# Kernel tuning notes

Hardware: AMD Instinct MI355X
Metric: run time of the kernel (lower is better)

## Reference

```python
import jax, jax.numpy as jnp
import numpy as np

EPS = 1e-5
SLOPE = 0.01  # LeakyReLU default negative_slope


def conv3(x, w):
    # x: [B,C,D,H,W], w: [O,I,3,3,3]; SubMConv3d on a dense grid == dense SAME conv, no bias
    return jax.lax.conv_general_dilated(
        x, w, window_strides=(1, 1, 1), padding='SAME',
        dimension_numbers=('NCDHW', 'OIDHW', 'NCDHW'))


def bn_c(x, g, b, m, v):
    # BatchNorm1d (eval) over channel axis 1 of [B,C,D,H,W]
    s = (1.0, -1, 1, 1, 1)
    return (x - m.reshape(1, -1, 1, 1, 1)) * (g.reshape(1, -1, 1, 1, 1) * jax.lax.rsqrt(v.reshape(1, -1, 1, 1, 1) + EPS)) + b.reshape(1, -1, 1, 1, 1)


def bn_f(x, g, b, m, v):
    # BatchNorm1d (eval) over last (feature) axis
    return (x - m) * (g * jax.lax.rsqrt(v + EPS)) + b


def lrelu(x):
    return jnp.where(x > 0, x, SLOPE * x)


def setup_inputs() -> dict:
    key = jax.random.key(0)
    ks = jax.random.split(key, 32)
    B, C, D, H, W = 2, 256, 64, 64, 16
    N = 100000
    init_size, emb = 32, 3

    fea = jax.random.normal(ks[0], (B, C, D, H, W), dtype=jnp.float32)
    gi0 = jax.random.randint(ks[1], (B, N), 0, D)
    gi1 = jax.random.randint(ks[2], (B, N), 0, H)
    gi2 = jax.random.randint(ks[3], (B, N), 0, W)
    grid_ind = jnp.stack([gi0, gi1, gi2], axis=-1).astype(jnp.int32)  # [B,N,3]
    xyz = jax.random.normal(ks[4], (B, N, 3), dtype=jnp.float32)

    def bn_params(k, c):
        k1, k2, k3, k4 = jax.random.split(k, 4)
        return (1.0 + 0.1 * jax.random.normal(k1, (c,), jnp.float32),
                0.1 * jax.random.normal(k2, (c,), jnp.float32),
                0.1 * jax.random.normal(k3, (c,), jnp.float32),
                0.5 + jax.random.uniform(k4, (c,), jnp.float32))

    W1 = jax.random.normal(ks[5], (C, C, 3, 3, 3), jnp.float32) * (1.0 / np.sqrt(27 * C))
    g1, b1, m1, v1 = bn_params(ks[6], C)
    W2 = jax.random.normal(ks[7], (2 * init_size, C, 3, 3, 3), jnp.float32) * (1.0 / np.sqrt(27 * C))
    g2, b2, m2, v2 = bn_params(ks[8], 2 * init_size)
    W3 = jax.random.normal(ks[9], (init_size, 2 * init_size, 3, 3, 3), jnp.float32) * (1.0 / np.sqrt(27 * 2 * init_size))
    g3, b3, m3, v3 = bn_params(ks[10], init_size)

    Wo1 = jax.random.normal(ks[11], (init_size + 3, init_size), jnp.float32) * (1.0 / np.sqrt(init_size + 3))
    bo1 = 0.01 * jax.random.normal(ks[12], (init_size,), jnp.float32)
    go, bo, mo, vo = bn_params(ks[13], init_size)
    Wo2 = jax.random.normal(ks[14], (init_size, emb), jnp.float32) * (1.0 / np.sqrt(init_size))
    bo2 = 0.01 * jax.random.normal(ks[15], (emb,), jnp.float32)

    return dict(fea=fea, grid_ind=grid_ind, xyz=xyz,
                W1=W1, g1=g1, b1=b1, m1=m1, v1=v1,
                W2=W2, g2=g2, b2=b2, m2=m2, v2=v2,
                W3=W3, g3=g3, b3=b3, m3=m3, v3=v3,
                Wo1=Wo1, bo1=bo1, go=go, bo=bo, mo=mo, vo=vo,
                Wo2=Wo2, bo2=bo2)


def reference(fea, grid_ind, xyz,
              W1, g1, b1, m1, v1,
              W2, g2, b2, m2, v2,
              W3, g3, b3, m3, v3,
              Wo1, bo1, go, bo, mo, vo,
              Wo2, bo2):
    # sparse conv stack (dense-grid equivalent)
    x = lrelu(bn_c(conv3(fea, W1), g1, b1, m1, v1))
    x = lrelu(bn_c(conv3(x, W2), g2, b2, m2, v2))
    x = lrelu(bn_c(conv3(x, W3), g3, b3, m3, v3))  # [B, init_size, D, H, W]

    # fea.dense().permute(0,2,3,4,1) -> [B, D, H, W, C]; per-point gather
    xg = jnp.transpose(x, (0, 2, 3, 4, 1))
    B = xg.shape[0]
    bidx = jnp.arange(B)[:, None]  # [B,1]
    pt = xg[bidx, grid_ind[:, :, 0], grid_ind[:, :, 1], grid_ind[:, :, 2]]  # [B, N, init_size]

    # concat xyz, Linear -> BN -> ReLU -> Linear
    h = jnp.concatenate([pt, xyz[:, :, :3]], axis=-1)
    h = jax.nn.relu(bn_f(h @ Wo1 + bo1, go, bo, mo, vo))
    return h @ Wo2 + bo2  # [B, N, embedding_dim]
```

## Files before the change

kernel.cpp:

```cpp
#include <hip/hip_runtime.h>
#include <stdint.h>

#define EPS 1e-5f
#define SLOPE 0.01f

typedef short bf16x8 __attribute__((ext_vector_type(8)));
typedef float f32x4 __attribute__((ext_vector_type(4)));

__device__ __forceinline__ uint16_t f2bf(float x) {
  union { float f; uint32_t u; } v; v.f = x;
  return (uint16_t)((v.u + 0x7fffu + ((v.u >> 16) & 1u)) >> 16);
}

__device__ __forceinline__ void g2lds16(const void* g, void* l) {
  __builtin_amdgcn_global_load_lds(
      (const __attribute__((address_space(1))) void*)g,
      (__attribute__((address_space(3))) void*)l, 16, 0, 0);
}

__global__ void prep_bn(const float* g1, const float* b1, const float* m1, const float* v1,
                        const float* g2, const float* b2, const float* m2, const float* v2,
                        const float* g3, const float* b3, const float* m3, const float* v3,
                        const float* go, const float* bo, const float* mo, const float* vo,
                        const float* bo1,
                        float* s1, float* be1, float* s2, float* be2,
                        float* s3, float* be3, float* so, float* beo) {
  int t = threadIdx.x;
  if (t < 256) { float s = g1[t] / sqrtf(v1[t] + EPS); s1[t] = s; be1[t] = b1[t] - m1[t] * s; }
  if (t < 64)  { float s = g2[t] / sqrtf(v2[t] + EPS); s2[t] = s; be2[t] = b2[t] - m2[t] * s; }
  if (t < 32)  { float s = g3[t] / sqrtf(v3[t] + EPS); s3[t] = s; be3[t] = b3[t] - m3[t] * s; }
  if (t < 32)  { float s = go[t] / sqrtf(vo[t] + EPS); so[t] = s; beo[t] = bo[t] + (bo1[t] - mo[t]) * s; }
}

__global__ void wtrans(const float* __restrict__ W, uint16_t* __restrict__ Wt,
                       int CO, int CI) {
  int idx = blockIdx.x * 256 + threadIdx.x;
  int total = CO * CI * 27;
  if (idx >= total) return;
  int t = idx / (CO * CI);
  int rem = idx % (CO * CI);
  int co = rem / CI, ci = rem % CI;
  Wt[idx] = f2bf(W[((size_t)co * CI + ci) * 27 + t]);
}

__global__ __launch_bounds__(256) void transpose_fea(const float* __restrict__ fea,
                                                     uint16_t* __restrict__ pad0) {
  int tid = threadIdx.x;
  int idx = blockIdx.x;
  int half = idx & 1;
  int q = (idx >> 1) & 3;
  int d = (idx >> 3) & 63;
  int b = idx >> 9;
  int s = q * 256 + tid;
  int h = s >> 4, w = s & 15;
  const float* src = fea + (size_t)(b * 256 + half * 128) * 65536 + (size_t)d * 1024 + s;
  uint16_t* dst = pad0 + ((size_t)b * 78408 +
                          (size_t)((d + 1) * 1188 + (h + 1) * 18 + (w + 1))) * 256 + half * 128;
#pragma unroll 4
  for (int c8 = 0; c8 < 16; ++c8) {
    uint16_t v[8];
#pragma unroll
    for (int j = 0; j < 8; ++j)
      v[j] = f2bf(src[(size_t)(c8 * 8 + j) * 65536]);
    *(uint4*)&dst[c8 * 8] = *(uint4*)v;
  }
}

template <int CI, int CO, int MH, int WM, int WN, bool LAST>
__global__ __launch_bounds__(256, 2) void conv_mfma(const uint16_t* __restrict__ padIn,
                                                    const uint16_t* __restrict__ Wt,
                                                    const float* __restrict__ bnS,
                                                    const float* __restrict__ bnB,
                                                    uint16_t* __restrict__ padOut,
                                                    float* __restrict__ x3out) {
  constexpr int NTILE = CO;
  constexpr int MTILE = MH * 16;
  constexpr int MPW = MTILE / WM;
  constexpr int NPW = NTILE / WN;
  constexpr int MSUB = MPW / 16;
  constexpr int NSUB = NPW / 16;
  constexpr int BPASS = NTILE / 32;
  constexpr int KC = CI / 64;
  constexpr int HB = 64 / MH;
  constexpr int HALF = MH / 8;
  constexpr int ROWSTR = 18 * CI;

  __shared__ __align__(16) uint16_t Alds[20 * MH * 64];
  __shared__ __align__(16) uint16_t Blds[NTILE * 64];

  const int tid = threadIdx.x;
  const int lane = tid & 63;
  const int wv = tid >> 6;
  const int wvm = wv / WN;
  const int wvn = wv % WN;

  const int mt = blockIdx.x;
  const int b = mt / (64 * HB);
  const int r = mt % (64 * HB);
  const int d = r / HB;
  const int h0 = (r % HB) * MH;

  const int subswB = (tid & 7) ^ ((tid >> 3) & 7);
  const int rowB0 = tid >> 3;

  f32x4 acc[MSUB][NSUB] = {};

  const size_t bOffIn = (size_t)b * 78408 * CI;

  for (int dh = 0; dh < 9; ++dh) {
    const int kd = dh / 3, kh = dh % 3;
    const size_t Abase = bOffIn + (size_t)((d + kd) * 1188 + (h0 + kh) * 18) * CI;
    for (int kc = 0; kc < KC; ++kc) {
      for (int kw = 0; kw < 3; ++kw) {
        __syncthreads();
        if (kw == 0) {
          const uint16_t* agBase = padIn + Abase + kc * 64 + (size_t)(lane >> 3) * ROWSTR;
#pragma unroll
          for (int p = 0; p < 5; ++p) {
            int wp = wv * 5 + p;
            int gu = (lane & 7) ^ (wp & 7);
#pragma unroll
            for (int hf = 0; hf < HALF; ++hf)
              g2lds16(agBase + (size_t)(hf * 8) * ROWSTR + wp * CI + gu * 8,
                      (char*)Alds + wp * (MH * 128) + hf * 1024);
          }
        }
        {
          const uint16_t* bg = Wt + (size_t)((dh * 3 + kw) * CO) * CI + kc * 64 + subswB * 8;
#pragma unroll
          for (int p = 0; p < BPASS; ++p)
            g2lds16(bg + (size_t)(rowB0 + 32 * p) * CI, (char*)Blds + p * 4096 + wv * 1024);
        }
        __syncthreads();
#pragma unroll
        for (int ks = 0; ks < 2; ++ks) {
          bf16x8 af[MSUB], bfr[NSUB];
#pragma unroll
          for (int mi = 0; mi < MSUB; ++mi) {
            int wq = (lane & 15) + kw;
            int u = (ks * 4 + (lane >> 4)) ^ (wq & 7);
            int mhIdx = wvm * MSUB + mi;
            af[mi] = *(const bf16x8*)&Alds[wq * (MH * 64) + mhIdx * 64 + u * 8];
          }
#pragma unroll
          for (int ni = 0; ni < NSUB; ++ni) {
            int row = wvn * NPW + ni * 16 + (lane & 15);
            int u = (ks * 4 + (lane >> 4)) ^ (row & 7);
            bfr[ni] = *(const bf16x8*)&Blds[row * 64 + u * 8];
          }
#pragma unroll
          for (int mi = 0; mi < MSUB; ++mi)
#pragma unroll
            for (int ni = 0; ni < NSUB; ++ni)
              acc[mi][ni] = __builtin_amdgcn_mfma_f32_16x16x32_bf16(af[mi], bfr[ni], acc[mi][ni], 0, 0, 0);
        }
      }
    }
  }

  const int col = lane & 15;
  const int quad = lane >> 4;
#pragma unroll
  for (int ni = 0; ni < NSUB; ++ni) {
    const int co = wvn * NPW + ni * 16 + col;
    const float sv = bnS[co];
    const float bv = bnB[co];
#pragma unroll
    for (int mi = 0; mi < MSUB; ++mi) {
#pragma unroll
      for (int rr = 0; rr < 4; ++rr) {
        int m = wvm * MPW + mi * 16 + quad * 4 + rr;
        float v = acc[mi][ni][rr] * sv + bv;
        v = v > 0.f ? v : SLOPE * v;
        int mh = m >> 4, w = m & 15;
        if (!LAST) {
          size_t o = ((size_t)b * 78408 +
                      (size_t)((d + 1) * 1188 + (h0 + mh + 1) * 18 + (w + 1))) * CO + co;
          padOut[o] = f2bf(v);
        } else {
          size_t o = ((size_t)b * 65536 + (size_t)((d * 64 + h0 + mh) * 16 + w)) * 32 + co;
          x3out[o] = v;
        }
      }
    }
  }
}

__global__ __launch_bounds__(256) void gather_mlp(const float* __restrict__ x3,
                                                  const int* __restrict__ gidx,
                                                  const float* __restrict__ xyz,
                                                  const float* __restrict__ Wo1,
                                                  const float* __restrict__ so,
                                                  const float* __restrict__ beo,
                                                  const float* __restrict__ Wo2,
                                                  const float* __restrict__ bo2,
                                                  float* __restrict__ out) {
  __shared__ __align__(16) float w1[35 * 32];
  __shared__ float w2[32 * 3];
  __shared__ float sS[32], sB[32], b2s[3];
  int tid = threadIdx.x;
  for (int i = tid; i < 1120; i += 256) w1[i] = Wo1[i];
  if (tid < 96) w2[tid] = Wo2[tid];
  if (tid < 32) { sS[tid] = so[tid]; sB[tid] = beo[tid]; }
  if (tid < 3) b2s[tid] = bo2[tid];
  __syncthreads();

  int idx = blockIdx.x * 256 + tid;
  if (idx >= 200000) return;
  int b = idx >= 100000 ? 1 : 0;
  int gb = idx * 3;
  int i0 = gidx[gb], i1 = gidx[gb + 1], i2 = gidx[gb + 2];
  const float* pt = x3 + ((size_t)b * 65536 + (size_t)((i0 * 64 + i1) * 16 + i2)) * 32;

  float h[35];
#pragma unroll
  for (int q = 0; q < 8; ++q) {
    float4 v = *(const float4*)(pt + q * 4);
    h[q * 4] = v.x; h[q * 4 + 1] = v.y; h[q * 4 + 2] = v.z; h[q * 4 + 3] = v.w;
  }
  h[32] = xyz[gb]; h[33] = xyz[gb + 1]; h[34] = xyz[gb + 2];

  float a[32];
#pragma unroll
  for (int j = 0; j < 32; ++j) a[j] = 0.f;
#pragma unroll
  for (int k = 0; k < 35; ++k) {
    float hk = h[k];
    const float4* wr = (const float4*)(w1 + k * 32);
#pragma unroll
    for (int q = 0; q < 8; ++q) {
      float4 wv = wr[q];
      a[q * 4 + 0] += hk * wv.x;
      a[q * 4 + 1] += hk * wv.y;
      a[q * 4 + 2] += hk * wv.z;
      a[q * 4 + 3] += hk * wv.w;
    }
  }
  float o0 = b2s[0], o1 = b2s[1], o2 = b2s[2];
#pragma unroll
  for (int j = 0; j < 32; ++j) {
    float y = a[j] * sS[j] + sB[j];
    y = y > 0.f ? y : 0.f;
    o0 += y * w2[j * 3 + 0];
    o1 += y * w2[j * 3 + 1];
    o2 += y * w2[j * 3 + 2];
  }
  out[gb] = o0; out[gb + 1] = o1; out[gb + 2] = o2;
}

extern "C" void kernel_launch(void* const* d_in, const int* in_sizes, int n_in,
                              void* d_out, int out_size, void* d_ws, size_t ws_size,
                              hipStream_t stream) {
  (void)in_sizes; (void)n_in; (void)out_size;
  if (ws_size < 165130000) return;

  const float* fea = (const float*)d_in[0];
  const int*   gidx = (const int*)d_in[1];
  const float* xyz = (const float*)d_in[2];
  const float* W1 = (const float*)d_in[3];
  const float* g1 = (const float*)d_in[4];
  const float* b1 = (const float*)d_in[5];
  const float* m1 = (const float*)d_in[6];
  const float* v1 = (const float*)d_in[7];
  const float* W2 = (const float*)d_in[8];
  const float* g2 = (const float*)d_in[9];
  const float* b2 = (const float*)d_in[10];
  const float* m2 = (const float*)d_in[11];
  const float* v2 = (const float*)d_in[12];
  const float* W3 = (const float*)d_in[13];
  const float* g3 = (const float*)d_in[14];
  const float* b3 = (const float*)d_in[15];
  const float* m3 = (const float*)d_in[16];
  const float* v3 = (const float*)d_in[17];
  const float* Wo1 = (const float*)d_in[18];
  const float* bo1 = (const float*)d_in[19];
  const float* go = (const float*)d_in[20];
  const float* bo = (const float*)d_in[21];
  const float* mo = (const float*)d_in[22];
  const float* vo = (const float*)d_in[23];
  const float* Wo2 = (const float*)d_in[24];
  const float* bo2 = (const float*)d_in[25];

  char* ws = (char*)d_ws;
  uint16_t* pad0 = (uint16_t*)(ws);
  uint16_t* pad1 = (uint16_t*)(ws + 80289792);
  uint16_t* Wt1 = (uint16_t*)(ws + 160579584);
  uint16_t* Wt2 = (uint16_t*)(ws + 164118528);
  uint16_t* Wt3 = (uint16_t*)(ws + 165003264);
  float* s1  = (float*)(ws + 165113856 + 0 * 1024);
  float* be1 = (float*)(ws + 165113856 + 1 * 1024);
  float* s2  = (float*)(ws + 165113856 + 2 * 1024);
  float* be2 = (float*)(ws + 165113856 + 3 * 1024);
  float* s3  = (float*)(ws + 165113856 + 4 * 1024);
  float* be3 = (float*)(ws + 165113856 + 5 * 1024);
  float* so  = (float*)(ws + 165113856 + 6 * 1024);
  float* beo = (float*)(ws + 165113856 + 7 * 1024);
  uint16_t* pad2 = (uint16_t*)(ws);
  float* x3 = (float*)(ws + 20072448);

  hipMemsetAsync(ws, 0, 160579584, stream);

  prep_bn<<<1, 256, 0, stream>>>(g1, b1, m1, v1, g2, b2, m2, v2, g3, b3, m3, v3,
                                 go, bo, mo, vo, bo1, s1, be1, s2, be2, s3, be3, so, beo);
  wtrans<<<6912, 256, 0, stream>>>(W1, Wt1, 256, 256);
  wtrans<<<1728, 256, 0, stream>>>(W2, Wt2, 64, 256);
  wtrans<<<216, 256, 0, stream>>>(W3, Wt3, 32, 64);
  transpose_fea<<<1024, 256, 0, stream>>>(fea, pad0);

  conv_mfma<256, 256, 8, 2, 2, false>
      <<<1024, 256, 0, stream>>>(pad0, Wt1, s1, be1, pad1, nullptr);

  hipMemsetAsync(pad2, 0, 20072448, stream);

  conv_mfma<256, 64, 16, 4, 1, false>
      <<<512, 256, 0, stream>>>(pad1, Wt2, s2, be2, pad2, nullptr);

  conv_mfma<64, 32, 16, 4, 1, true>
      <<<512, 256, 0, stream>>>(pad2, Wt3, s3, be3, nullptr, x3);

  gather_mlp<<<782, 256, 0, stream>>>(x3, gidx, xyz, Wo1, so, beo, Wo2, bo2, (float*)d_out);
}
```

Baseline: 1.048 ms.

## Double-buffer weight tiles in conv kernel and enlarge M tiles for later convs

```diff
diff --git a/kernel.cpp b/kernel.cpp
--- a/kernel.cpp
+++ b/kernel.cpp
@@ -67,7 +67,7 @@
 }
 
 template <int CI, int CO, int MH, int WM, int WN, bool LAST>
-__global__ __launch_bounds__(256, 2) void conv_mfma(const uint16_t* __restrict__ padIn,
+__global__ __launch_bounds__(256, 1) void conv_mfma(const uint16_t* __restrict__ padIn,
                                                     const uint16_t* __restrict__ Wt,
                                                     const float* __restrict__ bnS,
                                                     const float* __restrict__ bnB,
@@ -85,8 +85,8 @@
   constexpr int HALF = MH / 8;
   constexpr int ROWSTR = 18 * CI;
 
-  __shared__ __align__(16) uint16_t Alds[20 * MH * 64];
-  __shared__ __align__(16) uint16_t Blds[NTILE * 64];
+  __shared__ __align__(16) uint16_t Alds[18 * MH * 64];
+  __shared__ __align__(16) uint16_t Blds[2][NTILE * 64];
 
   const int tid = threadIdx.x;
   const int lane = tid & 63;
@@ -103,58 +103,86 @@
   const int subswB = (tid & 7) ^ ((tid >> 3) & 7);
   const int rowB0 = tid >> 3;
 
+  const size_t bOffIn = (size_t)b * 78408 * CI;
+
+  const int aslot0 = wv * 5 - (wv >= 2 ? (wv - 2) : 0);
+  const int anslots = (wv < 2) ? 5 : 4;
+
+  auto stageA = [&](int dh, int kc) {
+    const int kd = dh / 3, kh = dh % 3;
+    const uint16_t* agBase = padIn + bOffIn +
+        (size_t)((d + kd) * 1188 + (h0 + kh) * 18) * CI + kc * 64 +
+        (size_t)(lane >> 3) * ROWSTR;
+    for (int p = 0; p < anslots; ++p) {
+      int wp = aslot0 + p;
+      int gu = (lane & 7) ^ (wp & 7);
+#pragma unroll
+      for (int hf = 0; hf < HALF; ++hf)
+        g2lds16(agBase + (size_t)(hf * 8) * ROWSTR + wp * CI + gu * 8,
+                (char*)Alds + wp * (MH * 128) + hf * 1024);
+    }
+  };
+
+  auto stageB = [&](int dh, int kc, int kw, int sel) {
+    const uint16_t* bg = Wt + (size_t)((dh * 3 + kw) * CO) * CI + kc * 64 + subswB * 8;
+#pragma unroll
+    for (int p = 0; p < BPASS; ++p)
+      g2lds16(bg + (size_t)(rowB0 + 32 * p) * CI, (char*)Blds[sel] + p * 4096 + wv * 1024);
+  };
+
   f32x4 acc[MSUB][NSUB] = {};
 
-  const size_t bOffIn = (size_t)b * 78408 * CI;
-
+  auto compute = [&](int kw, int sel) {
+#pragma unroll
+    for (int ks = 0; ks < 2; ++ks) {
+      bf16x8 af[MSUB], bfr[NSUB];
+#pragma unroll
+      for (int mi = 0; mi < MSUB; ++mi) {
+        int wq = (lane & 15) + kw;
+        int u = (ks * 4 + (lane >> 4)) ^ (wq & 7);
+        int mhIdx = wvm * MSUB + mi;
+        af[mi] = *(const bf16x8*)&Alds[wq * (MH * 64) + mhIdx * 64 + u * 8];
+      }
+#pragma unroll
+      for (int ni = 0; ni < NSUB; ++ni) {
+        int row = wvn * NPW + ni * 16 + (lane & 15);
+        int u = (ks * 4 + (lane >> 4)) ^ (row & 7);
+        bfr[ni] = *(const bf16x8*)&Blds[sel][row * 64 + u * 8];
+      }
+#pragma unroll
+      for (int mi = 0; mi < MSUB; ++mi)
+#pragma unroll
+        for (int ni = 0; ni < NSUB; ++ni)
+          acc[mi][ni] = __builtin_amdgcn_mfma_f32_16x16x32_bf16(af[mi], bfr[ni], acc[mi][ni], 0, 0, 0);
+    }
+  };
+
+  stageA(0, 0);
+  stageB(0, 0, 0, 0);
+  __syncthreads();
+
+  int bsel = 0;
   for (int dh = 0; dh < 9; ++dh) {
-    const int kd = dh / 3, kh = dh % 3;
-    const size_t Abase = bOffIn + (size_t)((d + kd) * 1188 + (h0 + kh) * 18) * CI;
     for (int kc = 0; kc < KC; ++kc) {
-      for (int kw = 0; kw < 3; ++kw) {
+      const bool lastGroup = (dh == 8) && (kc == KC - 1);
+      stageB(dh, kc, 1, bsel ^ 1);
+      compute(0, bsel);
+      __syncthreads();
+      bsel ^= 1;
+      stageB(dh, kc, 2, bsel ^ 1);
+      compute(1, bsel);
+      __syncthreads();
+      bsel ^= 1;
+      const int dhn = (kc == KC - 1) ? dh + 1 : dh;
+      const int kcn = (kc == KC - 1) ? 0 : kc + 1;
+      if (!lastGroup) stageB(dhn, kcn, 0, bsel ^ 1);
+      compute(2, bsel);
+      __syncthreads();
+      if (!lastGroup) {
+        stageA(dhn, kcn);
         __syncthreads();
-        if (kw == 0) {
-          const uint16_t* agBase = padIn + Abase + kc * 64 + (size_t)(lane >> 3) * ROWSTR;
-#pragma unroll
-          for (int p = 0; p < 5; ++p) {
-            int wp = wv * 5 + p;
-            int gu = (lane & 7) ^ (wp & 7);
-#pragma unroll
-            for (int hf = 0; hf < HALF; ++hf)
-              g2lds16(agBase + (size_t)(hf * 8) * ROWSTR + wp * CI + gu * 8,
-                      (char*)Alds + wp * (MH * 128) + hf * 1024);
-          }
-        }
-        {
-          const uint16_t* bg = Wt + (size_t)((dh * 3 + kw) * CO) * CI + kc * 64 + subswB * 8;
-#pragma unroll
-          for (int p = 0; p < BPASS; ++p)
-            g2lds16(bg + (size_t)(rowB0 + 32 * p) * CI, (char*)Blds + p * 4096 + wv * 1024);
-        }
-        __syncthreads();
-#pragma unroll
-        for (int ks = 0; ks < 2; ++ks) {
-          bf16x8 af[MSUB], bfr[NSUB];
-#pragma unroll
-          for (int mi = 0; mi < MSUB; ++mi) {
-            int wq = (lane & 15) + kw;
-            int u = (ks * 4 + (lane >> 4)) ^ (wq & 7);
-            int mhIdx = wvm * MSUB + mi;
-            af[mi] = *(const bf16x8*)&Alds[wq * (MH * 64) + mhIdx * 64 + u * 8];
-          }
-#pragma unroll
-          for (int ni = 0; ni < NSUB; ++ni) {
-            int row = wvn * NPW + ni * 16 + (lane & 15);
-            int u = (ks * 4 + (lane >> 4)) ^ (row & 7);
-            bfr[ni] = *(const bf16x8*)&Blds[row * 64 + u * 8];
-          }
-#pragma unroll
-          for (int mi = 0; mi < MSUB; ++mi)
-#pragma unroll
-            for (int ni = 0; ni < NSUB; ++ni)
-              acc[mi][ni] = __builtin_amdgcn_mfma_f32_16x16x32_bf16(af[mi], bfr[ni], acc[mi][ni], 0, 0, 0);
-        }
       }
+      bsel ^= 1;
     }
   }
 
@@ -312,11 +340,11 @@
 
   hipMemsetAsync(pad2, 0, 20072448, stream);
 
-  conv_mfma<256, 64, 16, 4, 1, false>
-      <<<512, 256, 0, stream>>>(pad1, Wt2, s2, be2, pad2, nullptr);
-
-  conv_mfma<64, 32, 16, 4, 1, true>
-      <<<512, 256, 0, stream>>>(pad2, Wt3, s3, be3, nullptr, x3);
+  conv_mfma<256, 64, 32, 4, 1, false>
+      <<<256, 256, 0, stream>>>(pad1, Wt2, s2, be2, pad2, nullptr);
+
+  conv_mfma<64, 32, 32, 4, 1, true>
+      <<<256, 256, 0, stream>>>(pad2, Wt3, s3, be3, nullptr, x3);
 
   gather_mlp<<<782, 256, 0, stream>>>(x3, gidx, xyz, Wo1, so, beo, Wo2, bo2, (float*)d_out);
 }
```

Result: slower. 1.360 ms (+29.8%).

## Double-buffer A and B LDS tiles to overlap loads with MFMA compute

Applied to the files above, without the earlier changes.

```diff
diff --git a/kernel.cpp b/kernel.cpp
--- a/kernel.cpp
+++ b/kernel.cpp
@@ -79,20 +79,22 @@
   constexpr int NPW = NTILE / WN;
   constexpr int MSUB = MPW / 16;
   constexpr int NSUB = NPW / 16;
-  constexpr int BPASS = NTILE / 32;
   constexpr int KC = CI / 64;
+  constexpr int G = 9 * KC;
   constexpr int HB = 64 / MH;
   constexpr int HALF = MH / 8;
   constexpr int ROWSTR = 18 * CI;
 
-  __shared__ __align__(16) uint16_t Alds[20 * MH * 64];
-  __shared__ __align__(16) uint16_t Blds[NTILE * 64];
+  __shared__ __align__(16) uint16_t Alds[2][18 * MH * 64];
+  __shared__ __align__(16) uint16_t Blds[2][NTILE * 32];
 
   const int tid = threadIdx.x;
   const int lane = tid & 63;
   const int wv = tid >> 6;
   const int wvm = wv / WN;
   const int wvn = wv % WN;
+  const int col = lane & 15;
+  const int quad = lane >> 4;
 
   const int mt = blockIdx.x;
   const int b = mt / (64 * HB);
@@ -100,66 +102,88 @@
   const int d = r / HB;
   const int h0 = (r % HB) * MH;
 
-  const int subswB = (tid & 7) ^ ((tid >> 3) & 7);
-  const int rowB0 = tid >> 3;
+  const size_t bOffIn = (size_t)b * 78408 * CI;
+
+  const int qB = tid & 7;
+  const int rB = ((tid >> 3) << 1) + (qB >> 2);
+  const int uB = (qB & 3) ^ ((tid >> 3) & 3);
+
+  const int aslot0 = wv * 5 - (wv >= 2 ? (wv - 2) : 0);
+  const int anslots = (wv < 2) ? 5 : 4;
+
+  auto stageA = [&](int dh, int kc, int as) {
+    const int kd = dh / 3, kh = dh % 3;
+    const uint16_t* agBase = padIn + bOffIn +
+        (size_t)((d + kd) * 1188 + (h0 + kh) * 18) * CI + kc * 64 +
+        (size_t)(lane >> 3) * ROWSTR;
+    for (int p = 0; p < anslots; ++p) {
+      int wp = aslot0 + p;
+      int gu = (lane & 7) ^ (wp & 7);
+#pragma unroll
+      for (int hf = 0; hf < HALF; ++hf)
+        g2lds16(agBase + (size_t)(hf * 8) * ROWSTR + wp * CI + gu * 8,
+                (char*)Alds[as] + wp * (MH * 128) + hf * 1024);
+    }
+  };
+
+  auto stageB = [&](int dh, int kc, int kw, int ks) {
+    const uint16_t* bg = Wt + (size_t)((dh * 3 + kw) * CO) * CI + kc * 64 + ks * 32 + uB * 8;
+    if constexpr (CO >= 64) {
+#pragma unroll
+      for (int p = 0; p < CO / 64; ++p)
+        g2lds16(bg + (size_t)(rB + 64 * p) * CI, (char*)Blds[ks] + p * 4096 + wv * 1024);
+    } else {
+      if (tid < CO * 4)
+        g2lds16(bg + (size_t)rB * CI, (char*)Blds[ks] + wv * 1024);
+    }
+  };
 
   f32x4 acc[MSUB][NSUB] = {};
-
-  const size_t bOffIn = (size_t)b * 78408 * CI;
-
-  for (int dh = 0; dh < 9; ++dh) {
-    const int kd = dh / 3, kh = dh % 3;
-    const size_t Abase = bOffIn + (size_t)((d + kd) * 1188 + (h0 + kh) * 18) * CI;
-    for (int kc = 0; kc < KC; ++kc) {
-      for (int kw = 0; kw < 3; ++kw) {
-        __syncthreads();
-        if (kw == 0) {
-          const uint16_t* agBase = padIn + Abase + kc * 64 + (size_t)(lane >> 3) * ROWSTR;
-#pragma unroll
-          for (int p = 0; p < 5; ++p) {
-            int wp = wv * 5 + p;
-            int gu = (lane & 7) ^ (wp & 7);
-#pragma unroll
-            for (int hf = 0; hf < HALF; ++hf)
-              g2lds16(agBase + (size_t)(hf * 8) * ROWSTR + wp * CI + gu * 8,
-                      (char*)Alds + wp * (MH * 128) + hf * 1024);
-          }
-        }
-        {
-          const uint16_t* bg = Wt + (size_t)((dh * 3 + kw) * CO) * CI + kc * 64 + subswB * 8;
-#pragma unroll
-          for (int p = 0; p < BPASS; ++p)
-            g2lds16(bg + (size_t)(rowB0 + 32 * p) * CI, (char*)Blds + p * 4096 + wv * 1024);
-        }
-        __syncthreads();
-#pragma unroll
-        for (int ks = 0; ks < 2; ++ks) {
-          bf16x8 af[MSUB], bfr[NSUB];
-#pragma unroll
-          for (int mi = 0; mi < MSUB; ++mi) {
-            int wq = (lane & 15) + kw;
-            int u = (ks * 4 + (lane >> 4)) ^ (wq & 7);
-            int mhIdx = wvm * MSUB + mi;
-            af[mi] = *(const bf16x8*)&Alds[wq * (MH * 64) + mhIdx * 64 + u * 8];
-          }
-#pragma unroll
-          for (int ni = 0; ni < NSUB; ++ni) {
-            int row = wvn * NPW + ni * 16 + (lane & 15);
-            int u = (ks * 4 + (lane >> 4)) ^ (row & 7);
-            bfr[ni] = *(const bf16x8*)&Blds[row * 64 + u * 8];
-          }
-#pragma unroll
-          for (int mi = 0; mi < MSUB; ++mi)
-#pragma unroll
-            for (int ni = 0; ni < NSUB; ++ni)
-              acc[mi][ni] = __builtin_amdgcn_mfma_f32_16x16x32_bf16(af[mi], bfr[ni], acc[mi][ni], 0, 0, 0);
-        }
-      }
-    }
-  }
-
-  const int col = lane & 15;
-  const int quad = lane >> 4;
+  int acur = 0;
+
+  auto compute = [&](int kw, int ks) {
+    bf16x8 af[MSUB], bfr[NSUB];
+#pragma unroll
+    for (int mi = 0; mi < MSUB; ++mi) {
+      int wq = col + kw;
+      int u = (ks * 4 + quad) ^ (wq & 7);
+      int mhIdx = wvm * MSUB + mi;
+      af[mi] = *(const bf16x8*)&Alds[acur][wq * (MH * 64) + mhIdx * 64 + u * 8];
+    }
+#pragma unroll
+    for (int ni = 0; ni < NSUB; ++ni) {
+      int rw = wvn * NPW + ni * 16 + col;
+      int u = quad ^ ((rw >> 1) & 3);
+      bfr[ni] = *(const bf16x8*)&Blds[ks][(rw >> 1) * 64 + (rw & 1) * 32 + u * 8];
+    }
+#pragma unroll
+    for (int mi = 0; mi < MSUB; ++mi)
+#pragma unroll
+      for (int ni = 0; ni < NSUB; ++ni)
+        acc[mi][ni] = __builtin_amdgcn_mfma_f32_16x16x32_bf16(af[mi], bfr[ni], acc[mi][ni], 0, 0, 0);
+  };
+
+  stageA(0, 0, 0);
+  stageB(0, 0, 0, 0);
+  __syncthreads();
+
+  for (int g = 0; g < G; ++g) {
+    const int dh = g / KC, kc = g % KC;
+    const bool more = (g + 1 < G);
+    const int dhn = (kc == KC - 1) ? dh + 1 : dh;
+    const int kcn = (kc == KC - 1) ? 0 : kc + 1;
+#pragma unroll
+    for (int s = 0; s < 6; ++s) {
+      const int kw = s >> 1, ks = s & 1;
+      if (s < 5) stageB(dh, kc, (s + 1) >> 1, (s + 1) & 1);
+      else if (more) stageB(dhn, kcn, 0, 0);
+      if (s == 4 && more) stageA(dhn, kcn, acur ^ 1);
+      compute(kw, ks);
+      __syncthreads();
+    }
+    acur ^= 1;
+  }
+
 #pragma unroll
   for (int ni = 0; ni < NSUB; ++ni) {
     const int co = wvn * NPW + ni * 16 + col;
```

Result: slower. 1.133 ms (+8.1%).
